# Kernel optimization log

Hardware: AMD Instinct MI355X
Metric: run time of the kernel (lower is better)

Reference implementation:

```python
import jax, jax.numpy as jnp
import numpy as np

N = 65536   # nodes
D = 128     # in_dim == emb_dim (required by GRUCell usage)
E = 524288  # edges, pre-sorted by topological level
L = 8       # number of topological levels (edge_masks)


def _gru(x, h, Wi, Wh, bi, bh):
    # torch.nn.GRUCell semantics
    gi = x @ Wi.T + bi            # [*, 3D]
    gh = h @ Wh.T + bh
    ir, iz, i_n = jnp.split(gi, 3, axis=-1)
    hr, hz, h_n = jnp.split(gh, 3, axis=-1)
    r = jax.nn.sigmoid(ir + hr)
    z = jax.nn.sigmoid(iz + hz)
    n = jnp.tanh(i_n + r * h_n)
    return (1.0 - z) * n + z * h


def _direction(h_prev, j_lev, i_lev, ea_lev, We, be, Wa, ba, Wi, Wh, bi, bh):
    # j = message source (h_j gathered), i = aggregation target (segment index)
    n_nodes = h_prev.shape[0]
    # roots = nodes never appearing as aggregation target -> GRU with zero hidden
    root = ~jnp.zeros((n_nodes,), bool).at[i_lev.reshape(-1)].set(True)
    h = jnp.where(root[:, None], _gru(h_prev, jnp.zeros_like(h_prev), Wi, Wh, bi, bh), 0.0)

    def step(h, lev):
        j, i, ea = lev                       # [El], [El], [El, D]
        e = ea @ We.T + be                   # edge_lin
        q = h_prev[i]                        # h_prev_i
        k = h[j] + e                         # h_j + edge_emb
        v = h[j]
        alpha = (jnp.concatenate([q, k], axis=-1) @ Wa.T + ba)[:, 0]  # [El]
        # segment softmax over aggregation index i (numerically stable)
        m = jax.lax.stop_gradient(jax.ops.segment_max(alpha, i, num_segments=n_nodes))
        ex = jnp.exp(alpha - m[i])
        den = jax.ops.segment_sum(ex, i, num_segments=n_nodes)
        a = ex / den[i]
        msg = jax.ops.segment_sum(a[:, None] * v, i, num_segments=n_nodes)  # [N, D]
        mask = jnp.zeros((n_nodes,), bool).at[i].set(True)
        h_new = _gru(h_prev, msg, Wi, Wh, bi, bh)
        return jnp.where(mask[:, None], h_new, h), None

    h, _ = jax.lax.scan(step, h, (j_lev, i_lev, ea_lev))
    return h


def setup_inputs() -> dict:
    key = jax.random.key(0)
    ks = jax.random.split(key, 24)
    p = lambda k, shape: (0.05 * jax.random.normal(k, shape)).astype(jnp.float32)
    inp = {
        'x': jax.random.normal(ks[0], (N, D), jnp.float32),
        'edge_index': jax.random.randint(ks[1], (2, E), 0, N, dtype=jnp.int32),
        'edge_attr': jax.random.normal(ks[2], (E, D), jnp.float32),
        'num_levels': L,
        # forward-direction AttnConv + GRUCell params
        'We_f': p(ks[3], (D, D)), 'be_f': p(ks[4], (D,)),
        'Wa_f': p(ks[5], (1, 2 * D)), 'ba_f': p(ks[6], (1,)),
        'Wi_f': p(ks[7], (3 * D, D)), 'Wh_f': p(ks[8], (3 * D, D)),
        'bi_f': p(ks[9], (3 * D,)), 'bh_f': p(ks[10], (3 * D,)),
        # backward-direction params
        'We_b': p(ks[11], (D, D)), 'be_b': p(ks[12], (D,)),
        'Wa_b': p(ks[13], (1, 2 * D)), 'ba_b': p(ks[14], (1,)),
        'Wi_b': p(ks[15], (3 * D, D)), 'Wh_b': p(ks[16], (3 * D, D)),
        'bi_b': p(ks[17], (3 * D,)), 'bh_b': p(ks[18], (3 * D,)),
    }
    return inp


def reference(x, edge_index, edge_attr, num_levels,
              We_f, be_f, Wa_f, ba_f, Wi_f, Wh_f, bi_f, bh_f,
              We_b, be_b, Wa_b, ba_b, Wi_b, Wh_b, bi_b, bh_b):
    El = edge_index.shape[1] // num_levels
    src = edge_index[0].reshape(num_levels, El)
    dst = edge_index[1].reshape(num_levels, El)
    ea = edge_attr.reshape(num_levels, El, -1)
    # forward pass over levels: flow source->target, aggregate at dst
    h_fwd = _direction(x, src, dst, ea, We_f, be_f, Wa_f, ba_f, Wi_f, Wh_f, bi_f, bh_f)
    # fnb: backward pass takes h_fwd as h_prev; flow target->source (aggregate at src),
    # levels iterated in reverse
    h_bwd = _direction(h_fwd, dst[::-1], src[::-1], ea[::-1],
                       We_b, be_b, Wa_b, ba_b, Wi_b, Wh_b, bi_b, bh_b)
    return jax.nn.relu(h_bwd)
```

## Files before the change

kernel.cpp:

```cpp
#include <hip/hip_runtime.h>
#include <cstdint>
#include <cstddef>

constexpr int N_NODES = 65536;
constexpr int D       = 128;
constexpr int E_EDGES = 524288;
constexpr int LVLS    = 8;
constexpr int EL      = E_EDGES / LVLS;
constexpr int OSTR    = 65540;

typedef unsigned int  u32;
typedef unsigned short u16;
typedef __attribute__((ext_vector_type(8)))  short short8;
typedef __attribute__((ext_vector_type(16))) float f32x16;

__device__ __forceinline__ float sigmoidf_(float x) { return 1.0f / (1.0f + expf(-x)); }

__device__ __forceinline__ u32 bf_hi(float f) {
    u32 x = __float_as_uint(f);
    return (x + 0x7fffu + ((x >> 16) & 1u)) >> 16;
}
__device__ __forceinline__ float bf_f(u32 hbits) { return __uint_as_float(hbits << 16); }

__device__ __forceinline__ int swz(int row, int kbyte) {
    return row * 64 + (kbyte ^ ((row & 3) << 4));
}

__device__ __forceinline__ void gload_lds16(const void* g, void* l) {
    __builtin_amdgcn_global_load_lds(
        (const __attribute__((address_space(1))) unsigned int*)g,
        (__attribute__((address_space(3))) unsigned int*)l, 16, 0, 0);
}

__device__ __forceinline__ float wave_sum(float v) {
#pragma unroll
    for (int off = 32; off > 0; off >>= 1) v += __shfl_down(v, off, 64);
    return v;
}

__global__ __launch_bounds__(256)
void prep_kernel(const float* __restrict__ We_f, const float* __restrict__ Wa_f,
                 const float* __restrict__ be_f, const float* __restrict__ ba_f,
                 const float* __restrict__ We_b, const float* __restrict__ Wa_b,
                 const float* __restrict__ be_b, const float* __restrict__ ba_b,
                 float* __restrict__ u_f, float* __restrict__ u_b, float* __restrict__ cst)
{
    int t = threadIdx.x;
    if (t < 128) {
        float s = 0.f;
        for (int d = 0; d < 128; ++d) s = fmaf(We_f[d * 128 + t], Wa_f[128 + d], s);
        u_f[t] = s;
    } else {
        int c = t - 128;
        float s = 0.f;
        for (int d = 0; d < 128; ++d) s = fmaf(We_b[d * 128 + c], Wa_b[128 + d], s);
        u_b[c] = s;
    }
    if (t == 0) {
        float s = 0.f;
        for (int d = 0; d < 128; ++d) s = fmaf(be_f[d], Wa_f[128 + d], s);
        cst[0] = s + ba_f[0];
    }
    if (t == 255) {
        float s = 0.f;
        for (int d = 0; d < 128; ++d) s = fmaf(be_b[d], Wa_b[128 + d], s);
        cst[1] = s + ba_b[0];
    }
}

__global__ __launch_bounds__(256)
void convert_w(const float* __restrict__ W0, const float* __restrict__ W1,
               const float* __restrict__ W2, const float* __restrict__ W3,
               u16* __restrict__ hi4, u16* __restrict__ lo4)
{
    const float* Ws[4] = {W0, W1, W2, W3};
    int m = blockIdx.y;
    int i = blockIdx.x * 256 + threadIdx.x;
    int rw = i >> 7, k = i & 127;
    float v = Ws[m][i];
    u32 hb = bf_hi(v);
    hi4[(size_t)m * 49152 + i] = (u16)hb;
    if (rw >= 256)
        lo4[(size_t)m * 16384 + (size_t)(rw - 256) * 128 + k] = (u16)bf_hi(v - bf_f(hb));
}

__global__ __launch_bounds__(256)
void convert_x(const float* __restrict__ x, unsigned char* __restrict__ xhi,
               unsigned char* __restrict__ xlo)
{
    int idx = blockIdx.x * 256 + threadIdx.x;
    int n = idx >> 6, d = (idx & 63) << 1;
    float2 v = *reinterpret_cast<const float2*>(x + (size_t)n * 128 + d);
    u32 h0 = bf_hi(v.x), h1 = bf_hi(v.y);
    u32 l0 = bf_hi(v.x - bf_f(h0)), l1 = bf_hi(v.y - bf_f(h1));
    size_t off = (size_t)n * 256 + (size_t)d * 2;
    *reinterpret_cast<u32*>(xhi + off) = h0 | (h1 << 16);
    *reinterpret_cast<u32*>(xlo + off) = l0 | (l1 << 16);
}

__global__ __launch_bounds__(256)
void edot_kernel(const float* __restrict__ ea, const float* __restrict__ u_f,
                 const float* __restrict__ u_b, const float* __restrict__ cst,
                 float* __restrict__ edot_f, float* __restrict__ edot_b)
{
    int wv = threadIdx.x >> 6, lane = threadIdx.x & 63;
    int e = blockIdx.x * 4 + wv;
    if (e >= E_EDGES) return;
    int d = lane << 1;
    float2 v  = *reinterpret_cast<const float2*>(ea + (size_t)e * 128 + d);
    float2 uf = *reinterpret_cast<const float2*>(u_f + d);
    float2 ub = *reinterpret_cast<const float2*>(u_b + d);
    float af = wave_sum(v.x * uf.x + v.y * uf.y);
    float ab = wave_sum(v.x * ub.x + v.y * ub.y);
    if (lane == 0) {
        edot_f[e] = af + cst[0];
        edot_b[e] = ab + cst[1];
    }
}

__global__ __launch_bounds__(256)
void count_flags(const int* __restrict__ ei, int* __restrict__ counts,
                 int* __restrict__ flag_f, int* __restrict__ flag_b)
{
    int e = blockIdx.x * 256 + threadIdx.x;
    int lv = e >> 16;
    int s = ei[e], t = ei[E_EDGES + e];
    atomicAdd(&counts[(size_t)lv * 65536 + t], 1);
    atomicAdd(&counts[(size_t)(8 + lv) * 65536 + s], 1);
    flag_f[t] = 1;
    flag_b[s] = 1;
}

__global__ __launch_bounds__(1024)
void scan_compact(const int* __restrict__ counts, int* __restrict__ offs,
                  int* __restrict__ rows, int* __restrict__ cnts)
{
    __shared__ int sbuf[1024];
    __shared__ int nbuf[1024];
    int dl = blockIdx.x;
    const int4* c4 = reinterpret_cast<const int4*>(counts + (size_t)dl * 65536);
    int* o = offs + (size_t)dl * OSTR;
    int* rw = rows + (size_t)dl * 65536;
    int t = threadIdx.x;
    int cv[64];
#pragma unroll 4
    for (int k4 = 0; k4 < 16; ++k4) {
        int4 v = c4[t * 16 + k4];
        cv[k4 * 4 + 0] = v.x; cv[k4 * 4 + 1] = v.y;
        cv[k4 * 4 + 2] = v.z; cv[k4 * 4 + 3] = v.w;
    }
    int s = 0, nz = 0;
#pragma unroll
    for (int k = 0; k < 64; ++k) { s += cv[k]; nz += (cv[k] > 0); }
    sbuf[t] = s;
    nbuf[t] = nz;
    __syncthreads();
    int val = s, nval = nz;
    for (int off = 1; off < 1024; off <<= 1) {
        int add  = (t >= off) ? sbuf[t - off] : 0;
        int nadd = (t >= off) ? nbuf[t - off] : 0;
        __syncthreads();
        val += add;
        nval += nadd;
        sbuf[t] = val;
        nbuf[t] = nval;
        __syncthreads();
    }
    int run  = val - s;
    int nrun = nval - nz;
    int base = t * 64;
    int4* o4 = reinterpret_cast<int4*>(o + base);
#pragma unroll 4
    for (int k4 = 0; k4 < 16; ++k4) {
        int4 ov;
        ov.x = run; run += cv[k4 * 4 + 0];
        ov.y = run; run += cv[k4 * 4 + 1];
        ov.z = run; run += cv[k4 * 4 + 2];
        ov.w = run; run += cv[k4 * 4 + 3];
        o4[k4] = ov;
#pragma unroll
        for (int q = 0; q < 4; ++q)
            if (cv[k4 * 4 + q] > 0) rw[nrun++] = base + k4 * 4 + q;
    }
    if (t == 1023) { o[65536] = val; cnts[dl] = nval; }
}

__global__ __launch_bounds__(256)
void fill_csr(const int* __restrict__ ei, const float* __restrict__ edot_f,
              const float* __restrict__ edot_b, const int* __restrict__ offs,
              int* __restrict__ cursor, int2* __restrict__ csr)
{
    int idx = blockIdx.x * 256 + threadIdx.x;
    int dir = idx >= E_EDGES;
    int ge = dir ? idx - E_EDGES : idx;
    int lv = ge >> 16;
    int dl = dir * 8 + lv;
    int i = dir ? ei[ge] : ei[E_EDGES + ge];
    int j = dir ? ei[E_EDGES + ge] : ei[ge];
    int pos = offs[(size_t)dl * OSTR + i] + atomicAdd(&cursor[(size_t)dl * 65536 + i], 1);
    int2 v;
    v.x = j;
    v.y = __float_as_int(dir ? edot_b[ge] : edot_f[ge]);
    csr[(size_t)dl * EL + pos] = v;
}

__global__ __launch_bounds__(256)
void root_init(const float* __restrict__ hp, const int* __restrict__ flag,
               const float* __restrict__ Wi, const float* __restrict__ bi,
               const float* __restrict__ bh, const float* __restrict__ wa,
               float* __restrict__ h, unsigned char* __restrict__ h_hi,
               unsigned char* __restrict__ h_lo,
               float* __restrict__ qdot, float* __restrict__ hdot)
{
    int wv = threadIdx.x >> 6, lane = threadIdx.x & 63;
    int n = blockIdx.x * 4 + wv;
    int d = lane << 1;
    const float* hprow = hp + (size_t)n * 128;
    float2 hpv = *reinterpret_cast<const float2*>(hprow + d);
    float qd = wave_sum(hpv.x * wa[d] + hpv.y * wa[d + 1]);
    if (lane == 0) qdot[n] = qd;
    bool root = (flag[n] == 0);
    float hv[2] = {0.f, 0.f};
    if (root) {
#pragma unroll
        for (int q = 0; q < 2; ++q) {
            int dd = d + q;
            float g0 = bi[dd], g1 = bi[dd + 128], g2 = bi[dd + 256];
            for (int k = 0; k < 128; ++k) {
                float a = hprow[k];
                g0 = fmaf(a, Wi[(size_t)dd * 128 + k], g0);
                g1 = fmaf(a, Wi[(size_t)(dd + 128) * 128 + k], g1);
                g2 = fmaf(a, Wi[(size_t)(dd + 256) * 128 + k], g2);
            }
            float rr = sigmoidf_(g0 + bh[dd]);
            float zz = sigmoidf_(g1 + bh[dd + 128]);
            float nn = tanhf(g2 + rr * bh[dd + 256]);
            hv[q] = (1.f - zz) * nn;
        }
        *reinterpret_cast<float2*>(h + (size_t)n * 128 + d) = make_float2(hv[0], hv[1]);
        u32 hb0 = bf_hi(hv[0]), hb1 = bf_hi(hv[1]);
        u32 lb0 = bf_hi(hv[0] - bf_f(hb0)), lb1 = bf_hi(hv[1] - bf_f(hb1));
        size_t off = (size_t)n * 256 + (size_t)d * 2;
        *reinterpret_cast<u32*>(h_hi + off) = hb0 | (hb1 << 16);
        *reinterpret_cast<u32*>(h_lo + off) = lb0 | (lb1 << 16);
    }
    float hd = wave_sum(hv[0] * wa[128 + d] + hv[1] * wa[128 + d + 1]);
    if (lane == 0) hdot[n] = root ? hd : 0.f;
}

__global__ __launch_bounds__(256)
void attn_msg(const int* __restrict__ pcnt, const int* __restrict__ rows,
              const int* __restrict__ offs, const int2* __restrict__ csr,
              const float* __restrict__ qdot, const float* __restrict__ hdot,
              const float* __restrict__ h, unsigned char* __restrict__ msg_hi,
              unsigned char* __restrict__ msg_lo)
{
    int cnt = *pcnt;
    int l31 = threadIdx.x & 31;
    int hid = (blockIdx.x * 256 + threadIdx.x) >> 5;
    int nh = (gridDim.x * 256) >> 5;
    int d4 = l31 << 2;
    for (int r = hid; r < cnt; r += nh) {
        int i = rows[r];
        int o0 = offs[i], o1 = offs[i + 1];
        float qi = qdot[i];
        float den = 0.f;
        float4 acc = make_float4(0.f, 0.f, 0.f, 0.f);
        for (int e = o0; e < o1; ++e) {
            int2 je = csr[e];
            float ex = expf(qi + hdot[je.x] + __int_as_float(je.y));
            float4 hv = *reinterpret_cast<const float4*>(h + (size_t)je.x * 128 + d4);
            den += ex;
            acc.x = fmaf(ex, hv.x, acc.x);
            acc.y = fmaf(ex, hv.y, acc.y);
            acc.z = fmaf(ex, hv.z, acc.z);
            acc.w = fmaf(ex, hv.w, acc.w);
        }
        float inv = 1.f / den;
        float m0 = acc.x * inv, m1 = acc.y * inv, m2 = acc.z * inv, m3 = acc.w * inv;
        u32 h0 = bf_hi(m0), h1 = bf_hi(m1), h2 = bf_hi(m2), h3 = bf_hi(m3);
        u32 l0 = bf_hi(m0 - bf_f(h0)), l1 = bf_hi(m1 - bf_f(h1));
        u32 l2 = bf_hi(m2 - bf_f(h2)), l3 = bf_hi(m3 - bf_f(h3));
        size_t off = (size_t)r * 256 + (size_t)d4 * 2;
        *reinterpret_cast<uint2*>(msg_hi + off) = make_uint2(h0 | (h1 << 16), h2 | (h3 << 16));
        *reinterpret_cast<uint2*>(msg_lo + off) = make_uint2(l0 | (l1 << 16), l2 | (l3 << 16));
    }
}

__global__ __launch_bounds__(512, 1)
void gemm_gru(const unsigned char* __restrict__ msg_hi, const unsigned char* __restrict__ msg_lo,
              const unsigned char* __restrict__ hp_hi, const unsigned char* __restrict__ hp_lo,
              const u16* __restrict__ Whhi, const u16* __restrict__ Whlo,
              const u16* __restrict__ Wihi, const u16* __restrict__ Wilo,
              const int* __restrict__ pcnt, const int* __restrict__ rows,
              const float* __restrict__ bi, const float* __restrict__ bh,
              const float* __restrict__ wa,
              float* __restrict__ h, unsigned char* __restrict__ h_hi,
              unsigned char* __restrict__ h_lo, float* __restrict__ hdot)
{
    __shared__ __align__(16) unsigned char smem[32768 + 65536 + 2048 + 512];
    unsigned char* As = smem;
    unsigned char* Bs = smem + 32768;
    float* red   = (float*)(smem + 98304);
    int* rowsLds = (int*)(smem + 98304 + 2048);

    const int tid = threadIdx.x;
    const int cnt = *pcnt;
    const int row0 = blockIdx.x * 128;
    if (row0 >= cnt) return;

    if (tid < 128) {
        int gr = row0 + tid;
        rowsLds[tid] = (gr < cnt) ? rows[gr] : 0;
    }
    __syncthreads();

    const int lane = tid & 63, wv = tid >> 6;
    const int q = wv & 3, mh = wv >> 2;
    const int l31 = lane & 31, l5 = lane >> 5;

    const int rwA = wv * 16 + (lane >> 2);
    const int slA = ((lane & 3) << 4) ^ ((rwA & 3) << 4);
    const size_t baseA0 = (size_t)(row0 + rwA) * 256 + slA;
    const size_t baseA1 = (size_t)rowsLds[rwA] * 256 + slA;
    size_t bsrc[3];
#pragma unroll
    for (int k = 0; k < 3; ++k) {
        int rwB = wv * 48 + k * 16 + (lane >> 2);
        bsrc[k] = (size_t)rwB * 256 + (((lane & 3) << 4) ^ ((rwB & 3) << 4));
    }
    const int rwL = wv * 16 + (lane >> 2);
    const size_t lsrc = (size_t)rwL * 256 + (((lane & 3) << 4) ^ ((rwL & 3) << 4));

    f32x16 acc[2][3];
#pragma unroll
    for (int mt = 0; mt < 2; ++mt)
#pragma unroll
        for (int g = 0; g < 3; ++g) acc[mt][g] = (f32x16)0.0f;
    f32x16 ghn[2];

    auto STAGE = [&](int t, int b) {
        int ph = t >> 2, ks = t & 3;
        size_t ko = (size_t)ks * 64;
        const unsigned char* Ahi = ph ? hp_hi : msg_hi;
        const unsigned char* Alo = ph ? hp_lo : msg_lo;
        size_t ab = (ph ? baseA1 : baseA0) + ko;
        unsigned char* Ad = As + b * 16384 + wv * 1024;
        gload_lds16(Ahi + ab, Ad);
        gload_lds16(Alo + ab, Ad + 8192);
        const unsigned char* Bh = (const unsigned char*)(ph ? Wihi : Whhi);
        const unsigned char* Bl = (const unsigned char*)(ph ? Wilo : Whlo);
        unsigned char* Bd = Bs + b * 32768;
#pragma unroll
        for (int k = 0; k < 3; ++k)
            gload_lds16(Bh + bsrc[k] + ko, Bd + (wv * 3 + k) * 1024);
        gload_lds16(Bl + lsrc + ko, Bd + 24576 + wv * 1024);
    };

    STAGE(0, 0);
    for (int t = 0; t < 8; ++t) {
        int b = t & 1;
        if (t < 7) STAGE(t + 1, b ^ 1);
        __builtin_amdgcn_sched_barrier(0);
        if (t < 7) asm volatile("s_waitcnt vmcnt(6)");
        else       asm volatile("s_waitcnt vmcnt(0)");
        __builtin_amdgcn_s_barrier();
        __builtin_amdgcn_sched_barrier(0);

        const unsigned char* Ab = As + b * 16384;
        const unsigned char* Bb = Bs + b * 32768;
#pragma unroll
        for (int kh = 0; kh < 2; ++kh) {
            short8 a[2][2];
#pragma unroll
            for (int mt = 0; mt < 2; ++mt)
#pragma unroll
                for (int hf = 0; hf < 2; ++hf)
                    a[mt][hf] = *reinterpret_cast<const short8*>(
                        Ab + hf * 8192 + swz(mh * 64 + mt * 32 + l31, kh * 32 + l5 * 16));
            short8 b0 = *reinterpret_cast<const short8*>(
                Bb + swz(q * 32 + l31, kh * 32 + l5 * 16));
            short8 b1 = *reinterpret_cast<const short8*>(
                Bb + swz(q * 32 + 128 + l31, kh * 32 + l5 * 16));
            short8 b2 = *reinterpret_cast<const short8*>(
                Bb + swz(q * 32 + 256 + l31, kh * 32 + l5 * 16));
            short8 bl2 = *reinterpret_cast<const short8*>(
                Bb + 24576 + swz(q * 32 + l31, kh * 32 + l5 * 16));
#pragma unroll
            for (int mt = 0; mt < 2; ++mt) {
                acc[mt][0] = __builtin_amdgcn_mfma_f32_32x32x16_bf16(a[mt][0], b0, acc[mt][0], 0, 0, 0);
                acc[mt][0] = __builtin_amdgcn_mfma_f32_32x32x16_bf16(a[mt][1], b0, acc[mt][0], 0, 0, 0);
                acc[mt][1] = __builtin_amdgcn_mfma_f32_32x32x16_bf16(a[mt][0], b1, acc[mt][1], 0, 0, 0);
                acc[mt][1] = __builtin_amdgcn_mfma_f32_32x32x16_bf16(a[mt][1], b1, acc[mt][1], 0, 0, 0);
                acc[mt][2] = __builtin_amdgcn_mfma_f32_32x32x16_bf16(a[mt][0], b2, acc[mt][2], 0, 0, 0);
                acc[mt][2] = __builtin_amdgcn_mfma_f32_32x32x16_bf16(a[mt][0], bl2, acc[mt][2], 0, 0, 0);
                acc[mt][2] = __builtin_amdgcn_mfma_f32_32x32x16_bf16(a[mt][1], b2, acc[mt][2], 0, 0, 0);
            }
        }
        if (t == 3) {
            ghn[0] = acc[0][2];
            ghn[1] = acc[1][2];
            acc[0][2] = (f32x16)0.0f;
            acc[1][2] = (f32x16)0.0f;
        }
        __builtin_amdgcn_s_barrier();
        __builtin_amdgcn_sched_barrier(0);
    }

    const int d = q * 32 + l31;
    const float wa2d = wa[128 + d];
    const float bi0 = bi[d], bi1 = bi[d + 128], bi2 = bi[d + 256];
    const float bh0 = bh[d], bh1 = bh[d + 128], bh2 = bh[d + 256];

#pragma unroll
    for (int mt = 0; mt < 2; ++mt)
#pragma unroll
        for (int rg = 0; rg < 16; ++rg) {
            int rl = mh * 64 + mt * 32 + (rg & 3) + ((rg >> 2) << 3) + (l5 << 2);
            int gr = row0 + rl;
            bool ok = gr < cnt;
            int n = rowsLds[rl];
            u16 mhb = *reinterpret_cast<const u16*>(msg_hi + (size_t)gr * 256 + (size_t)d * 2);
            u16 mlb = *reinterpret_cast<const u16*>(msg_lo + (size_t)gr * 256 + (size_t)d * 2);
            float mval = bf_f(mhb) + bf_f(mlb);
            float rr = sigmoidf_(acc[mt][0][rg] + bi0 + bh0);
            float zz = sigmoidf_(acc[mt][1][rg] + bi1 + bh1);
            float nn = tanhf(acc[mt][2][rg] + bi2 + rr * (ghn[mt][rg] + bh2));
            float hv = (1.f - zz) * nn + zz * mval;
            if (ok) {
                h[(size_t)n * 128 + d] = hv;
                u32 hb = bf_hi(hv);
                *reinterpret_cast<u16*>(h_hi + (size_t)n * 256 + (size_t)d * 2) = (u16)hb;
                *reinterpret_cast<u16*>(h_lo + (size_t)n * 256 + (size_t)d * 2) =
                    (u16)bf_hi(hv - bf_f(hb));
            }
            float pd = hv * wa2d;
#pragma unroll
            for (int o = 1; o < 32; o <<= 1) pd += __shfl_xor(pd, o, 64);
            if (l31 == 0) red[rl * 4 + q] = pd;
        }
    __syncthreads();
    if (tid < 128 && row0 + tid < cnt) {
        int n = rowsLds[tid];
        hdot[n] = red[tid * 4] + red[tid * 4 + 1] + red[tid * 4 + 2] + red[tid * 4 + 3];
    }
}

__global__ __launch_bounds__(256)
void relu_kernel(const float* __restrict__ h, float* __restrict__ out)
{
    int idx = (blockIdx.x * 256 + threadIdx.x) * 4;
    float4 v = *reinterpret_cast<const float4*>(h + idx);
    v.x = fmaxf(v.x, 0.f); v.y = fmaxf(v.y, 0.f);
    v.z = fmaxf(v.z, 0.f); v.w = fmaxf(v.w, 0.f);
    *reinterpret_cast<float4*>(out + idx) = v;
}

extern "C" void kernel_launch(void* const* d_in, const int* in_sizes, int n_in,
                              void* d_out, int out_size, void* d_ws, size_t ws_size,
                              hipStream_t stream)
{
    (void)in_sizes; (void)n_in; (void)out_size; (void)ws_size;

    const float* x    = (const float*)d_in[0];
    const int*   ei   = (const int*)d_in[1];
    const float* ea   = (const float*)d_in[2];
    const float* We_f = (const float*)d_in[4];
    const float* be_f = (const float*)d_in[5];
    const float* Wa_f = (const float*)d_in[6];
    const float* ba_f = (const float*)d_in[7];
    const float* Wi_f = (const float*)d_in[8];
    const float* Wh_f = (const float*)d_in[9];
    const float* bi_f = (const float*)d_in[10];
    const float* bh_f = (const float*)d_in[11];
    const float* We_b = (const float*)d_in[12];
    const float* be_b = (const float*)d_in[13];
    const float* Wa_b = (const float*)d_in[14];
    const float* ba_b = (const float*)d_in[15];
    const float* Wi_b = (const float*)d_in[16];
    const float* Wh_b = (const float*)d_in[17];
    const float* bi_b = (const float*)d_in[18];
    const float* bh_b = (const float*)d_in[19];
    float* out = (float*)d_out;

    char* p = (char*)d_ws;
    auto carve = [&](size_t bytes) -> char* {
        char* r = p;
        p += (bytes + 255) & ~(size_t)255;
        return r;
    };
    int*   counts  = (int*)carve((size_t)16 * 65536 * 4);
    int*   cursor  = (int*)carve((size_t)16 * 65536 * 4);
    int*   flag_f  = (int*)carve((size_t)N_NODES * 4);
    int*   flag_b  = (int*)carve((size_t)N_NODES * 4);
    float* h_fwd   = (float*)carve((size_t)N_NODES * D * 4);
    float* h_cur   = (float*)carve((size_t)N_NODES * D * 4);
    unsigned char* hf_hi = (unsigned char*)carve((size_t)N_NODES * 256);
    unsigned char* hf_lo = (unsigned char*)carve((size_t)N_NODES * 256);
    size_t zbytes  = (size_t)((char*)hf_lo - (char*)counts) + (size_t)N_NODES * 256;
    int*   cnts    = (int*)carve(256);
    u16*   Whi4    = (u16*)carve((size_t)4 * 49152 * 2);
    u16*   Wlo4    = (u16*)carve((size_t)4 * 16384 * 2);
    unsigned char* x_hi  = (unsigned char*)carve((size_t)N_NODES * 256);
    unsigned char* x_lo  = (unsigned char*)carve((size_t)N_NODES * 256);
    unsigned char* hc_hi = (unsigned char*)carve((size_t)N_NODES * 256);
    unsigned char* hc_lo = (unsigned char*)carve((size_t)N_NODES * 256);
    unsigned char* msg_hi= (unsigned char*)carve((size_t)N_NODES * 256);
    unsigned char* msg_lo= (unsigned char*)carve((size_t)N_NODES * 256);
    float* u_f     = (float*)carve((size_t)D * 4);
    float* u_b     = (float*)carve((size_t)D * 4);
    float* cst     = (float*)carve(16);
    float* edot_f  = (float*)carve((size_t)E_EDGES * 4);
    float* edot_b  = (float*)carve((size_t)E_EDGES * 4);
    int*   offs    = (int*)carve((size_t)16 * OSTR * 4);
    int2*  csr     = (int2*)carve((size_t)16 * EL * 8);
    int*   rows    = (int*)carve((size_t)16 * 65536 * 4);
    float* qdot    = (float*)carve((size_t)N_NODES * 4);
    float* hdot    = (float*)carve((size_t)N_NODES * 4);

    hipMemsetAsync(counts, 0, zbytes, stream);
    prep_kernel<<<1, 256, 0, stream>>>(We_f, Wa_f, be_f, ba_f, We_b, Wa_b, be_b, ba_b,
                                       u_f, u_b, cst);
    convert_w<<<dim3(192, 4), 256, 0, stream>>>(Wi_f, Wh_f, Wi_b, Wh_b, Whi4, Wlo4);
    convert_x<<<16384, 256, 0, stream>>>(x, x_hi, x_lo);
    count_flags<<<E_EDGES / 256, 256, 0, stream>>>(ei, counts, flag_f, flag_b);
    edot_kernel<<<E_EDGES / 4, 256, 0, stream>>>(ea, u_f, u_b, cst, edot_f, edot_b);
    scan_compact<<<16, 1024, 0, stream>>>(counts, offs, rows, cnts);
    fill_csr<<<2 * E_EDGES / 256, 256, 0, stream>>>(ei, edot_f, edot_b, offs, cursor, csr);

    for (int dir = 0; dir < 2; ++dir) {
        const float* hp   = dir == 0 ? x : h_fwd;
        float*       h    = dir == 0 ? h_fwd : h_cur;
        const unsigned char* hp_hi = dir == 0 ? x_hi : hf_hi;
        const unsigned char* hp_lo = dir == 0 ? x_lo : hf_lo;
        unsigned char* h_hi = dir == 0 ? hf_hi : hc_hi;
        unsigned char* h_lo = dir == 0 ? hf_lo : hc_lo;
        const u16* Wihi = Whi4 + (size_t)(dir * 2) * 49152;
        const u16* Whhi = Whi4 + (size_t)(dir * 2 + 1) * 49152;
        const u16* Wilo = Wlo4 + (size_t)(dir * 2) * 16384;
        const u16* Whlo = Wlo4 + (size_t)(dir * 2 + 1) * 16384;
        const float* Wi   = dir == 0 ? Wi_f : Wi_b;
        const float* bi   = dir == 0 ? bi_f : bi_b;
        const float* bh   = dir == 0 ? bh_f : bh_b;
        const float* wa   = dir == 0 ? Wa_f : Wa_b;
        const int*   flag = dir == 0 ? flag_f : flag_b;

        root_init<<<N_NODES / 4, 256, 0, stream>>>(hp, flag, Wi, bi, bh, wa,
                                                   h, h_hi, h_lo, qdot, hdot);

        for (int t = 0; t < LVLS; ++t) {
            int lv = dir == 0 ? t : (LVLS - 1 - t);
            int dl = dir * LVLS + lv;
            attn_msg<<<2048, 256, 0, stream>>>(
                cnts + dl, rows + (size_t)dl * 65536, offs + (size_t)dl * OSTR,
                csr + (size_t)dl * EL, qdot, hdot, h, msg_hi, msg_lo);
            gemm_gru<<<512, 512, 0, stream>>>(
                msg_hi, msg_lo, hp_hi, hp_lo, Whhi, Whlo, Wihi, Wilo,
                cnts + dl, rows + (size_t)dl * 65536,
                bi, bh, wa, h, h_hi, h_lo, hdot);
        }
    }
    relu_kernel<<<(N_NODES * D) / 1024, 256, 0, stream>>>(h_cur, out);
}
```

Before: 1.702 ms.

## Drop low-bf16 message/weight terms, retile GRU GEMM, fuse edge count kernels

Messages are now stored only as high bf16, and the Wh low-part correction MFMAs are removed, so the msg@Wh product uses single bf16 precision and the split-precision terms stay only on the hp@Wi side. The GRU GEMM is retiled from 128-row/512-thread blocks to 64-row/256-thread blocks with two blocks per CU, and the per-block row LDS cache is dropped. The count/flag work is folded into the edot kernel, and the attention loop software-prefetches the next CSR entry. The backward direction also skips writing bf16 images it never reads. The bf16-only message path lowers accuracy and may exceed tolerance.

```diff
diff --git a/kernel.cpp b/kernel.cpp
--- a/kernel.cpp
+++ b/kernel.cpp
@@ -99,9 +99,12 @@
 }
 
 __global__ __launch_bounds__(256)
-void edot_kernel(const float* __restrict__ ea, const float* __restrict__ u_f,
-                 const float* __restrict__ u_b, const float* __restrict__ cst,
-                 float* __restrict__ edot_f, float* __restrict__ edot_b)
+void edot_count(const float* __restrict__ ea, const float* __restrict__ u_f,
+                const float* __restrict__ u_b, const float* __restrict__ cst,
+                const int* __restrict__ ei,
+                float* __restrict__ edot_f, float* __restrict__ edot_b,
+                int* __restrict__ counts, int* __restrict__ flag_f,
+                int* __restrict__ flag_b)
 {
     int wv = threadIdx.x >> 6, lane = threadIdx.x & 63;
     int e = blockIdx.x * 4 + wv;
@@ -115,20 +118,13 @@
     if (lane == 0) {
         edot_f[e] = af + cst[0];
         edot_b[e] = ab + cst[1];
-    }
-}
-
-__global__ __launch_bounds__(256)
-void count_flags(const int* __restrict__ ei, int* __restrict__ counts,
-                 int* __restrict__ flag_f, int* __restrict__ flag_b)
-{
-    int e = blockIdx.x * 256 + threadIdx.x;
-    int lv = e >> 16;
-    int s = ei[e], t = ei[E_EDGES + e];
-    atomicAdd(&counts[(size_t)lv * 65536 + t], 1);
-    atomicAdd(&counts[(size_t)(8 + lv) * 65536 + s], 1);
-    flag_f[t] = 1;
-    flag_b[s] = 1;
+        int lv = e >> 16;
+        int s = ei[e], t = ei[E_EDGES + e];
+        atomicAdd(&counts[(size_t)lv * 65536 + t], 1);
+        atomicAdd(&counts[(size_t)(8 + lv) * 65536 + s], 1);
+        flag_f[t] = 1;
+        flag_b[s] = 1;
+    }
 }
 
 __global__ __launch_bounds__(1024)
@@ -209,7 +205,7 @@
                const float* __restrict__ Wi, const float* __restrict__ bi,
                const float* __restrict__ bh, const float* __restrict__ wa,
                float* __restrict__ h, unsigned char* __restrict__ h_hi,
-               unsigned char* __restrict__ h_lo,
+               unsigned char* __restrict__ h_lo, int write_img,
                float* __restrict__ qdot, float* __restrict__ hdot)
 {
     int wv = threadIdx.x >> 6, lane = threadIdx.x & 63;
@@ -238,11 +234,13 @@
             hv[q] = (1.f - zz) * nn;
         }
         *reinterpret_cast<float2*>(h + (size_t)n * 128 + d) = make_float2(hv[0], hv[1]);
-        u32 hb0 = bf_hi(hv[0]), hb1 = bf_hi(hv[1]);
-        u32 lb0 = bf_hi(hv[0] - bf_f(hb0)), lb1 = bf_hi(hv[1] - bf_f(hb1));
-        size_t off = (size_t)n * 256 + (size_t)d * 2;
-        *reinterpret_cast<u32*>(h_hi + off) = hb0 | (hb1 << 16);
-        *reinterpret_cast<u32*>(h_lo + off) = lb0 | (lb1 << 16);
+        if (write_img) {
+            u32 hb0 = bf_hi(hv[0]), hb1 = bf_hi(hv[1]);
+            u32 lb0 = bf_hi(hv[0] - bf_f(hb0)), lb1 = bf_hi(hv[1] - bf_f(hb1));
+            size_t off = (size_t)n * 256 + (size_t)d * 2;
+            *reinterpret_cast<u32*>(h_hi + off) = hb0 | (hb1 << 16);
+            *reinterpret_cast<u32*>(h_lo + off) = lb0 | (lb1 << 16);
+        }
     }
     float hd = wave_sum(hv[0] * wa[128 + d] + hv[1] * wa[128 + d + 1]);
     if (lane == 0) hdot[n] = root ? hd : 0.f;
@@ -252,8 +250,7 @@
 void attn_msg(const int* __restrict__ pcnt, const int* __restrict__ rows,
               const int* __restrict__ offs, const int2* __restrict__ csr,
               const float* __restrict__ qdot, const float* __restrict__ hdot,
-              const float* __restrict__ h, unsigned char* __restrict__ msg_hi,
-              unsigned char* __restrict__ msg_lo)
+              const float* __restrict__ h, unsigned char* __restrict__ msg_hi)
 {
     int cnt = *pcnt;
     int l31 = threadIdx.x & 31;
@@ -266,8 +263,10 @@
         float qi = qdot[i];
         float den = 0.f;
         float4 acc = make_float4(0.f, 0.f, 0.f, 0.f);
+        int2 je = csr[o0];
         for (int e = o0; e < o1; ++e) {
-            int2 je = csr[e];
+            int en = e + 1;
+            int2 jn = (en < o1) ? csr[en] : je;
             float ex = expf(qi + hdot[je.x] + __int_as_float(je.y));
             float4 hv = *reinterpret_cast<const float4*>(h + (size_t)je.x * 128 + d4);
             den += ex;
@@ -275,62 +274,59 @@
             acc.y = fmaf(ex, hv.y, acc.y);
             acc.z = fmaf(ex, hv.z, acc.z);
             acc.w = fmaf(ex, hv.w, acc.w);
+            je = jn;
         }
         float inv = 1.f / den;
-        float m0 = acc.x * inv, m1 = acc.y * inv, m2 = acc.z * inv, m3 = acc.w * inv;
-        u32 h0 = bf_hi(m0), h1 = bf_hi(m1), h2 = bf_hi(m2), h3 = bf_hi(m3);
-        u32 l0 = bf_hi(m0 - bf_f(h0)), l1 = bf_hi(m1 - bf_f(h1));
-        u32 l2 = bf_hi(m2 - bf_f(h2)), l3 = bf_hi(m3 - bf_f(h3));
-        size_t off = (size_t)r * 256 + (size_t)d4 * 2;
-        *reinterpret_cast<uint2*>(msg_hi + off) = make_uint2(h0 | (h1 << 16), h2 | (h3 << 16));
-        *reinterpret_cast<uint2*>(msg_lo + off) = make_uint2(l0 | (l1 << 16), l2 | (l3 << 16));
-    }
-}
-
-__global__ __launch_bounds__(512, 1)
-void gemm_gru(const unsigned char* __restrict__ msg_hi, const unsigned char* __restrict__ msg_lo,
+        u32 h0 = bf_hi(acc.x * inv), h1 = bf_hi(acc.y * inv);
+        u32 h2 = bf_hi(acc.z * inv), h3 = bf_hi(acc.w * inv);
+        *reinterpret_cast<uint2*>(msg_hi + (size_t)r * 256 + (size_t)d4 * 2) =
+            make_uint2(h0 | (h1 << 16), h2 | (h3 << 16));
+    }
+}
+
+__global__ __launch_bounds__(256, 2)
+void gemm_gru(const unsigned char* __restrict__ msg_hi,
               const unsigned char* __restrict__ hp_hi, const unsigned char* __restrict__ hp_lo,
-              const u16* __restrict__ Whhi, const u16* __restrict__ Whlo,
+              const u16* __restrict__ Whhi,
               const u16* __restrict__ Wihi, const u16* __restrict__ Wilo,
               const int* __restrict__ pcnt, const int* __restrict__ rows,
               const float* __restrict__ bi, const float* __restrict__ bh,
               const float* __restrict__ wa,
               float* __restrict__ h, unsigned char* __restrict__ h_hi,
-              unsigned char* __restrict__ h_lo, float* __restrict__ hdot)
-{
-    __shared__ __align__(16) unsigned char smem[32768 + 65536 + 2048 + 512];
+              unsigned char* __restrict__ h_lo, int write_img,
+              float* __restrict__ hdot)
+{
+    __shared__ __align__(16) unsigned char smem[16384 + 65536];
     unsigned char* As = smem;
-    unsigned char* Bs = smem + 32768;
-    float* red   = (float*)(smem + 98304);
-    int* rowsLds = (int*)(smem + 98304 + 2048);
+    unsigned char* Bs = smem + 16384;
 
     const int tid = threadIdx.x;
     const int cnt = *pcnt;
-    const int row0 = blockIdx.x * 128;
+    const int row0 = blockIdx.x * 64;
     if (row0 >= cnt) return;
 
-    if (tid < 128) {
-        int gr = row0 + tid;
-        rowsLds[tid] = (gr < cnt) ? rows[gr] : 0;
-    }
-    __syncthreads();
-
     const int lane = tid & 63, wv = tid >> 6;
-    const int q = wv & 3, mh = wv >> 2;
+    const int q = wv;
     const int l31 = lane & 31, l5 = lane >> 5;
 
     const int rwA = wv * 16 + (lane >> 2);
     const int slA = ((lane & 3) << 4) ^ ((rwA & 3) << 4);
-    const size_t baseA0 = (size_t)(row0 + rwA) * 256 + slA;
-    const size_t baseA1 = (size_t)rowsLds[rwA] * 256 + slA;
-    size_t bsrc[3];
-#pragma unroll
-    for (int k = 0; k < 3; ++k) {
-        int rwB = wv * 48 + k * 16 + (lane >> 2);
+    int garA = row0 + rwA;
+    const size_t baseA0 = (size_t)garA * 256 + slA;
+    int rowA1 = rows[garA < cnt ? garA : 0];
+    const size_t baseA1 = (size_t)rowA1 * 256 + slA;
+    size_t bsrc[6];
+#pragma unroll
+    for (int k = 0; k < 6; ++k) {
+        int rwB = wv * 96 + k * 16 + (lane >> 2);
         bsrc[k] = (size_t)rwB * 256 + (((lane & 3) << 4) ^ ((rwB & 3) << 4));
     }
-    const int rwL = wv * 16 + (lane >> 2);
-    const size_t lsrc = (size_t)rwL * 256 + (((lane & 3) << 4) ^ ((rwL & 3) << 4));
+    size_t lsrc[2];
+#pragma unroll
+    for (int k = 0; k < 2; ++k) {
+        int rwL = wv * 32 + k * 16 + (lane >> 2);
+        lsrc[k] = (size_t)rwL * 256 + (((lane & 3) << 4) ^ ((rwL & 3) << 4));
+    }
 
     f32x16 acc[2][3];
 #pragma unroll
@@ -339,62 +335,77 @@
         for (int g = 0; g < 3; ++g) acc[mt][g] = (f32x16)0.0f;
     f32x16 ghn[2];
 
-    auto STAGE = [&](int t, int b) {
-        int ph = t >> 2, ks = t & 3;
-        size_t ko = (size_t)ks * 64;
-        const unsigned char* Ahi = ph ? hp_hi : msg_hi;
-        const unsigned char* Alo = ph ? hp_lo : msg_lo;
-        size_t ab = (ph ? baseA1 : baseA0) + ko;
-        unsigned char* Ad = As + b * 16384 + wv * 1024;
-        gload_lds16(Ahi + ab, Ad);
-        gload_lds16(Alo + ab, Ad + 8192);
-        const unsigned char* Bh = (const unsigned char*)(ph ? Wihi : Whhi);
-        const unsigned char* Bl = (const unsigned char*)(ph ? Wilo : Whlo);
+    auto STAGE = [&](int tt) {
+        int b = tt & 1;
+        size_t ko = (size_t)(tt & 3) * 64;
         unsigned char* Bd = Bs + b * 32768;
-#pragma unroll
-        for (int k = 0; k < 3; ++k)
-            gload_lds16(Bh + bsrc[k] + ko, Bd + (wv * 3 + k) * 1024);
-        gload_lds16(Bl + lsrc + ko, Bd + 24576 + wv * 1024);
+        if (tt < 4) {
+            gload_lds16(msg_hi + baseA0 + ko, As + b * 8192 + wv * 1024);
+#pragma unroll
+            for (int k = 0; k < 6; ++k)
+                gload_lds16((const unsigned char*)Whhi + bsrc[k] + ko, Bd + (wv * 6 + k) * 1024);
+        } else {
+            gload_lds16(hp_hi + baseA1 + ko, As + b * 8192 + wv * 1024);
+            gload_lds16(hp_lo + baseA1 + ko, As + b * 8192 + 4096 + wv * 1024);
+#pragma unroll
+            for (int k = 0; k < 6; ++k)
+                gload_lds16((const unsigned char*)Wihi + bsrc[k] + ko, Bd + (wv * 6 + k) * 1024);
+#pragma unroll
+            for (int k = 0; k < 2; ++k)
+                gload_lds16((const unsigned char*)Wilo + lsrc[k] + ko, Bd + 24576 + (wv * 2 + k) * 1024);
+        }
     };
 
-    STAGE(0, 0);
+    STAGE(0);
     for (int t = 0; t < 8; ++t) {
-        int b = t & 1;
-        if (t < 7) STAGE(t + 1, b ^ 1);
+        if (t < 7) STAGE(t + 1);
         __builtin_amdgcn_sched_barrier(0);
-        if (t < 7) asm volatile("s_waitcnt vmcnt(6)");
-        else       asm volatile("s_waitcnt vmcnt(0)");
+        if (t < 3)      asm volatile("s_waitcnt vmcnt(7)");
+        else if (t < 7) asm volatile("s_waitcnt vmcnt(10)");
+        else            asm volatile("s_waitcnt vmcnt(0)");
         __builtin_amdgcn_s_barrier();
         __builtin_amdgcn_sched_barrier(0);
 
-        const unsigned char* Ab = As + b * 16384;
-        const unsigned char* Bb = Bs + b * 32768;
+        const unsigned char* Ab = As + (t & 1) * 8192;
+        const unsigned char* Bb = Bs + (t & 1) * 32768;
 #pragma unroll
         for (int kh = 0; kh < 2; ++kh) {
-            short8 a[2][2];
-#pragma unroll
-            for (int mt = 0; mt < 2; ++mt)
-#pragma unroll
-                for (int hf = 0; hf < 2; ++hf)
-                    a[mt][hf] = *reinterpret_cast<const short8*>(
-                        Ab + hf * 8192 + swz(mh * 64 + mt * 32 + l31, kh * 32 + l5 * 16));
             short8 b0 = *reinterpret_cast<const short8*>(
                 Bb + swz(q * 32 + l31, kh * 32 + l5 * 16));
             short8 b1 = *reinterpret_cast<const short8*>(
                 Bb + swz(q * 32 + 128 + l31, kh * 32 + l5 * 16));
             short8 b2 = *reinterpret_cast<const short8*>(
                 Bb + swz(q * 32 + 256 + l31, kh * 32 + l5 * 16));
-            short8 bl2 = *reinterpret_cast<const short8*>(
-                Bb + 24576 + swz(q * 32 + l31, kh * 32 + l5 * 16));
-#pragma unroll
-            for (int mt = 0; mt < 2; ++mt) {
-                acc[mt][0] = __builtin_amdgcn_mfma_f32_32x32x16_bf16(a[mt][0], b0, acc[mt][0], 0, 0, 0);
-                acc[mt][0] = __builtin_amdgcn_mfma_f32_32x32x16_bf16(a[mt][1], b0, acc[mt][0], 0, 0, 0);
-                acc[mt][1] = __builtin_amdgcn_mfma_f32_32x32x16_bf16(a[mt][0], b1, acc[mt][1], 0, 0, 0);
-                acc[mt][1] = __builtin_amdgcn_mfma_f32_32x32x16_bf16(a[mt][1], b1, acc[mt][1], 0, 0, 0);
-                acc[mt][2] = __builtin_amdgcn_mfma_f32_32x32x16_bf16(a[mt][0], b2, acc[mt][2], 0, 0, 0);
-                acc[mt][2] = __builtin_amdgcn_mfma_f32_32x32x16_bf16(a[mt][0], bl2, acc[mt][2], 0, 0, 0);
-                acc[mt][2] = __builtin_amdgcn_mfma_f32_32x32x16_bf16(a[mt][1], b2, acc[mt][2], 0, 0, 0);
+            short8 ah[2];
+#pragma unroll
+            for (int mt = 0; mt < 2; ++mt)
+                ah[mt] = *reinterpret_cast<const short8*>(
+                    Ab + swz(mt * 32 + l31, kh * 32 + l5 * 16));
+            if (t < 4) {
+#pragma unroll
+                for (int mt = 0; mt < 2; ++mt) {
+                    acc[mt][0] = __builtin_amdgcn_mfma_f32_32x32x16_bf16(ah[mt], b0, acc[mt][0], 0, 0, 0);
+                    acc[mt][1] = __builtin_amdgcn_mfma_f32_32x32x16_bf16(ah[mt], b1, acc[mt][1], 0, 0, 0);
+                    acc[mt][2] = __builtin_amdgcn_mfma_f32_32x32x16_bf16(ah[mt], b2, acc[mt][2], 0, 0, 0);
+                }
+            } else {
+                short8 bl2 = *reinterpret_cast<const short8*>(
+                    Bb + 24576 + swz(q * 32 + l31, kh * 32 + l5 * 16));
+                short8 al[2];
+#pragma unroll
+                for (int mt = 0; mt < 2; ++mt)
+                    al[mt] = *reinterpret_cast<const short8*>(
+                        Ab + 4096 + swz(mt * 32 + l31, kh * 32 + l5 * 16));
+#pragma unroll
+                for (int mt = 0; mt < 2; ++mt) {
+                    acc[mt][0] = __builtin_amdgcn_mfma_f32_32x32x16_bf16(ah[mt], b0, acc[mt][0], 0, 0, 0);
+                    acc[mt][0] = __builtin_amdgcn_mfma_f32_32x32x16_bf16(al[mt], b0, acc[mt][0], 0, 0, 0);
+                    acc[mt][1] = __builtin_amdgcn_mfma_f32_32x32x16_bf16(ah[mt], b1, acc[mt][1], 0, 0, 0);
+                    acc[mt][1] = __builtin_amdgcn_mfma_f32_32x32x16_bf16(al[mt], b1, acc[mt][1], 0, 0, 0);
+                    acc[mt][2] = __builtin_amdgcn_mfma_f32_32x32x16_bf16(ah[mt], b2, acc[mt][2], 0, 0, 0);
+                    acc[mt][2] = __builtin_amdgcn_mfma_f32_32x32x16_bf16(ah[mt], bl2, acc[mt][2], 0, 0, 0);
+                    acc[mt][2] = __builtin_amdgcn_mfma_f32_32x32x16_bf16(al[mt], b2, acc[mt][2], 0, 0, 0);
+                }
             }
         }
         if (t == 3) {
@@ -407,6 +418,8 @@
         __builtin_amdgcn_sched_barrier(0);
     }
 
+    __syncthreads();
+    float* red = (float*)Bs;
     const int d = q * 32 + l31;
     const float wa2d = wa[128 + d];
     const float bi0 = bi[d], bi1 = bi[d + 128], bi2 = bi[d + 256];
@@ -416,23 +429,24 @@
     for (int mt = 0; mt < 2; ++mt)
 #pragma unroll
         for (int rg = 0; rg < 16; ++rg) {
-            int rl = mh * 64 + mt * 32 + (rg & 3) + ((rg >> 2) << 3) + (l5 << 2);
+            int rl = mt * 32 + (rg & 3) + ((rg >> 2) << 3) + (l5 << 2);
             int gr = row0 + rl;
             bool ok = gr < cnt;
-            int n = rowsLds[rl];
-            u16 mhb = *reinterpret_cast<const u16*>(msg_hi + (size_t)gr * 256 + (size_t)d * 2);
-            u16 mlb = *reinterpret_cast<const u16*>(msg_lo + (size_t)gr * 256 + (size_t)d * 2);
-            float mval = bf_f(mhb) + bf_f(mlb);
+            int n = rows[ok ? gr : 0];
+            float mval = bf_f(*reinterpret_cast<const u16*>(
+                msg_hi + (size_t)gr * 256 + (size_t)d * 2));
             float rr = sigmoidf_(acc[mt][0][rg] + bi0 + bh0);
             float zz = sigmoidf_(acc[mt][1][rg] + bi1 + bh1);
             float nn = tanhf(acc[mt][2][rg] + bi2 + rr * (ghn[mt][rg] + bh2));
             float hv = (1.f - zz) * nn + zz * mval;
             if (ok) {
                 h[(size_t)n * 128 + d] = hv;
-                u32 hb = bf_hi(hv);
-                *reinterpret_cast<u16*>(h_hi + (size_t)n * 256 + (size_t)d * 2) = (u16)hb;
-                *reinterpret_cast<u16*>(h_lo + (size_t)n * 256 + (size_t)d * 2) =
-                    (u16)bf_hi(hv - bf_f(hb));
+                if (write_img) {
+                    u32 hb = bf_hi(hv);
+                    *reinterpret_cast<u16*>(h_hi + (size_t)n * 256 + (size_t)d * 2) = (u16)hb;
+                    *reinterpret_cast<u16*>(h_lo + (size_t)n * 256 + (size_t)d * 2) =
+                        (u16)bf_hi(hv - bf_f(hb));
+                }
             }
             float pd = hv * wa2d;
 #pragma unroll
@@ -440,8 +454,8 @@
             if (l31 == 0) red[rl * 4 + q] = pd;
         }
     __syncthreads();
-    if (tid < 128 && row0 + tid < cnt) {
-        int n = rowsLds[tid];
+    if (tid < 64 && row0 + tid < cnt) {
+        int n = rows[row0 + tid];
         hdot[n] = red[tid * 4] + red[tid * 4 + 1] + red[tid * 4 + 2] + red[tid * 4 + 3];
     }
 }
@@ -495,18 +509,15 @@
     int*   flag_b  = (int*)carve((size_t)N_NODES * 4);
     float* h_fwd   = (float*)carve((size_t)N_NODES * D * 4);
     float* h_cur   = (float*)carve((size_t)N_NODES * D * 4);
+    size_t zbytes  = (size_t)((char*)h_cur - (char*)counts) + (size_t)N_NODES * D * 4;
     unsigned char* hf_hi = (unsigned char*)carve((size_t)N_NODES * 256);
     unsigned char* hf_lo = (unsigned char*)carve((size_t)N_NODES * 256);
-    size_t zbytes  = (size_t)((char*)hf_lo - (char*)counts) + (size_t)N_NODES * 256;
     int*   cnts    = (int*)carve(256);
     u16*   Whi4    = (u16*)carve((size_t)4 * 49152 * 2);
     u16*   Wlo4    = (u16*)carve((size_t)4 * 16384 * 2);
     unsigned char* x_hi  = (unsigned char*)carve((size_t)N_NODES * 256);
     unsigned char* x_lo  = (unsigned char*)carve((size_t)N_NODES * 256);
-    unsigned char* hc_hi = (unsigned char*)carve((size_t)N_NODES * 256);
-    unsigned char* hc_lo = (unsigned char*)carve((size_t)N_NODES * 256);
     unsigned char* msg_hi= (unsigned char*)carve((size_t)N_NODES * 256);
-    unsigned char* msg_lo= (unsigned char*)carve((size_t)N_NODES * 256);
     float* u_f     = (float*)carve((size_t)D * 4);
     float* u_b     = (float*)carve((size_t)D * 4);
     float* cst     = (float*)carve(16);
@@ -523,8 +534,8 @@
                                        u_f, u_b, cst);
     convert_w<<<dim3(192, 4), 256, 0, stream>>>(Wi_f, Wh_f, Wi_b, Wh_b, Whi4, Wlo4);
     convert_x<<<16384, 256, 0, stream>>>(x, x_hi, x_lo);
-    count_flags<<<E_EDGES / 256, 256, 0, stream>>>(ei, counts, flag_f, flag_b);
-    edot_kernel<<<E_EDGES / 4, 256, 0, stream>>>(ea, u_f, u_b, cst, edot_f, edot_b);
+    edot_count<<<E_EDGES / 4, 256, 0, stream>>>(ea, u_f, u_b, cst, ei,
+                                                edot_f, edot_b, counts, flag_f, flag_b);
     scan_compact<<<16, 1024, 0, stream>>>(counts, offs, rows, cnts);
     fill_csr<<<2 * E_EDGES / 256, 256, 0, stream>>>(ei, edot_f, edot_b, offs, cursor, csr);
 
@@ -533,12 +544,12 @@
         float*       h    = dir == 0 ? h_fwd : h_cur;
         const unsigned char* hp_hi = dir == 0 ? x_hi : hf_hi;
         const unsigned char* hp_lo = dir == 0 ? x_lo : hf_lo;
-        unsigned char* h_hi = dir == 0 ? hf_hi : hc_hi;
-        unsigned char* h_lo = dir == 0 ? hf_lo : hc_lo;
+        unsigned char* h_hi = hf_hi;
+        unsigned char* h_lo = hf_lo;
+        int write_img = (dir == 0);
         const u16* Wihi = Whi4 + (size_t)(dir * 2) * 49152;
         const u16* Whhi = Whi4 + (size_t)(dir * 2 + 1) * 49152;
         const u16* Wilo = Wlo4 + (size_t)(dir * 2) * 16384;
-        const u16* Whlo = Wlo4 + (size_t)(dir * 2 + 1) * 16384;
         const float* Wi   = dir == 0 ? Wi_f : Wi_b;
         const float* bi   = dir == 0 ? bi_f : bi_b;
         const float* bh   = dir == 0 ? bh_f : bh_b;
@@ -546,18 +557,18 @@
         const int*   flag = dir == 0 ? flag_f : flag_b;
 
         root_init<<<N_NODES / 4, 256, 0, stream>>>(hp, flag, Wi, bi, bh, wa,
-                                                   h, h_hi, h_lo, qdot, hdot);
+                                                   h, h_hi, h_lo, write_img, qdot, hdot);
 
         for (int t = 0; t < LVLS; ++t) {
             int lv = dir == 0 ? t : (LVLS - 1 - t);
             int dl = dir * LVLS + lv;
             attn_msg<<<2048, 256, 0, stream>>>(
                 cnts + dl, rows + (size_t)dl * 65536, offs + (size_t)dl * OSTR,
-                csr + (size_t)dl * EL, qdot, hdot, h, msg_hi, msg_lo);
-            gemm_gru<<<512, 512, 0, stream>>>(
-                msg_hi, msg_lo, hp_hi, hp_lo, Whhi, Whlo, Wihi, Wilo,
+                csr + (size_t)dl * EL, qdot, hdot, h, msg_hi);
+            gemm_gru<<<1024, 256, 0, stream>>>(
+                msg_hi, hp_hi, hp_lo, Whhi, Wihi, Wilo,
                 cnts + dl, rows + (size_t)dl * 65536,
-                bi, bh, wa, h, h_hi, h_lo, hdot);
+                bi, bh, wa, h, h_hi, h_lo, write_img, hdot);
         }
     }
     relu_kernel<<<(N_NODES * D) / 1024, 256, 0, stream>>>(h_cur, out);
```

New measurement: 1.480 ms. -13.1%, faster.
